# Kernel tuning notes

Hardware: AMD Instinct MI355X
Metric: run time of the kernel (lower is better)

The kernel has to match this reference:

```python
import jax, jax.numpy as jnp
import numpy as np

EPS = 1e-6
PC_MIN = jnp.array([-50.0, -50.0, -4.0], jnp.float32)
PC_MAX = jnp.array([50.0, 50.0, 4.0], jnp.float32)
IMG_H, IMG_W = 256, 704
G, P, L, D = 1, 8, 4, 128


def _conv3x3(x, w, b):
    y = jax.lax.conv_general_dilated(x, w, (1, 1), ((1, 1), (1, 1)),
                                     dimension_numbers=('NCHW', 'OIHW', 'NCHW'))
    return y + b[None, :, None, None]


def _inorm(x):
    # InstanceNorm2d(affine=False), eps=1e-5, per-sample per-channel over (H,W)
    m = jnp.mean(x, axis=(2, 3), keepdims=True)
    v = jnp.var(x, axis=(2, 3), keepdims=True)
    return (x - m) * jax.lax.rsqrt(v + 1e-5)


def _bilinear(img, xy):
    # img: [H, W, C]; xy: [M, 2] in [0,1] (align_corners=False, zero padding)
    H, W, _ = img.shape
    px = xy[:, 0] * W - 0.5
    py = xy[:, 1] * H - 0.5
    x0 = jnp.floor(px)
    y0 = jnp.floor(py)
    wx = px - x0
    wy = py - y0
    x0 = x0.astype(jnp.int32)
    y0 = y0.astype(jnp.int32)

    def tap(xi, yi, w):
        ok = (xi >= 0) & (xi < W) & (yi >= 0) & (yi < H)
        v = img[jnp.clip(yi, 0, H - 1), jnp.clip(xi, 0, W - 1)]
        return v * (w * ok)[:, None]

    return (tap(x0, y0, (1 - wx) * (1 - wy)) + tap(x0 + 1, y0, wx * (1 - wy)) +
            tap(x0, y0 + 1, (1 - wx) * wy) + tap(x0 + 1, y0 + 1, wx * wy))


def _sampling_4d(pts, feats, scale_w, l2i):
    # pts: [B,Q,G,P,3]; feats: list of [B*G,N,Hl,Wl,C]; scale_w: [B,Q,G,1,P,L]; l2i: [B,N,4,4]
    B, Q, g, p, _ = pts.shape
    N = l2i.shape[1]
    hom = jnp.concatenate([pts, jnp.ones(pts.shape[:-1] + (1,), pts.dtype)], -1)
    cam = jnp.einsum('bnij,bqgpj->bqngpi', l2i, hom)  # project to each camera
    z = cam[..., 2:3]
    xy = cam[..., :2] / jnp.maximum(z, 1e-5)
    xy = xy / jnp.array([IMG_W, IMG_H], xy.dtype)
    xy = jnp.where(z > 1e-5, xy, -1e4)  # behind camera -> samples zero
    xy = jnp.transpose(xy, (0, 3, 2, 1, 4, 5)).reshape(B * g * N, Q * p, 2)
    out = 0.0
    for l, f in enumerate(feats):
        C = f.shape[-1]
        fi = f.reshape(B * g * N, f.shape[2], f.shape[3], C)
        s = jax.vmap(_bilinear)(fi, xy).reshape(B, g, N, Q, p, C).sum(2)  # sum over cameras
        w = jnp.transpose(scale_w[:, :, :, 0, :, l], (0, 2, 1, 3))  # [B,G,Q,P]
        out = out + s * w[..., None]
    return jnp.transpose(out, (0, 2, 1, 3, 4))  # [B,Q,G,P,C]


def _forward(feat0, feat1, feat2, feat3, lidar2img, bev_query, bev_pos,
             in_w, in_b, off_w, off_b, sw_w, sw_b,
             pe_w1, pe_b1, pe_w2, pe_b2,
             mid_w1, mid_b1, mid_w2, mid_b2, mid_w3, mid_b3,
             out_w, out_b):
    B, _, h, w = bev_query.shape
    # decoder prologue: b n (g c) H W -> (b g) n H W c  (G=1)
    feats = [jnp.transpose(f, (0, 1, 3, 4, 2)) for f in (feat0, feat1, feat2, feat3)]
    q = _inorm(bev_query + _conv3x3(bev_query, in_w, in_b))
    qf = jnp.transpose(q, (0, 2, 3, 1)).reshape(B, h * w, D)
    # sampling offsets (1x1 conv as matmul), mode='grid', scale=1.0
    off = jax.nn.sigmoid(qf @ off_w.T + off_b).reshape(B, h * w, G, P, 3)
    lim_xy = 0.25 * 1.0 + EPS
    lim_z = 4.0 + EPS
    off = jnp.concatenate([off[..., :2] * 2 * lim_xy - lim_xy,
                           off[..., 2:3] * 2 * lim_z - lim_z], -1)
    ref = bev_pos.reshape(B, h * w, 1, 1, 3) * (PC_MAX - PC_MIN) + PC_MIN
    pts = ref + off  # [B,Q,G,P,3] in world coords
    sw = (qf @ sw_w.T + sw_b).reshape(B, h * w, G, P, L)[:, :, :, None]  # b q g 1 p l
    sw = jax.nn.softmax(sw, axis=-1)
    sampled = _sampling_4d(pts, feats, sw, lidar2img)  # [B,Q,G,P,128]
    ref_n = (pts - PC_MIN) / (PC_MAX - PC_MIN)
    pe = jax.nn.relu(ref_n @ pe_w1 + pe_b1) @ pe_w2 + pe_b2  # PositionalEncodingMap MLP
    sampled = sampled + pe
    # b (h w) g p c -> b (p g c) h w
    sf = jnp.transpose(sampled, (0, 3, 2, 4, 1)).reshape(B, P * G * 128, h, w)
    m = jax.nn.gelu(jnp.einsum('oi,bihw->bohw', mid_w1, sf) + mid_b1[None, :, None, None], approximate=False)
    m = jax.nn.gelu(jnp.einsum('oi,bihw->bohw', mid_w2, m) + mid_b2[None, :, None, None], approximate=False)
    m = jnp.einsum('oi,bihw->bohw', mid_w3, m) + mid_b3[None, :, None, None]
    q = _inorm(q + m)
    q = _inorm(q + _conv3x3(q, out_w, out_b))
    height = jnp.transpose(off[..., 2], (0, 2, 3, 1)).reshape(B, G, P, h, w)
    return q, height


def _lidar2img_np():
    mats = []
    K = np.array([[500., 0., IMG_W / 2, 0.],
                  [0., 500., IMG_H / 2, 0.],
                  [0., 0., 1., 0.],
                  [0., 0., 0., 1.]])
    for n in range(6):
        th = 2 * np.pi * n / 6
        fwd = np.array([np.cos(th), np.sin(th), 0.])
        right = np.array([-np.sin(th), np.cos(th), 0.])
        down = np.array([0., 0., -1.])
        R = np.stack([right, down, fwd])
        c = fwd * 0.5 + np.array([0., 0., 1.5])
        T = np.eye(4)
        T[:3, :3] = R
        T[:3, 3] = -R @ c
        mats.append(K @ T)
    return np.stack(mats)[None].astype(np.float32)


def setup_inputs():
    key = jax.random.key(0)
    ks = jax.random.split(key, 16)

    def rn(k, shape, s=0.02):
        return jax.random.normal(k, shape, jnp.float32) * s

    B, N, h, w = 1, 6, 128, 128
    return dict(
        feat0=jax.random.normal(ks[0], (B, N, 128, 32, 88), jnp.float32),
        feat1=jax.random.normal(ks[1], (B, N, 128, 16, 44), jnp.float32),
        feat2=jax.random.normal(ks[2], (B, N, 128, 8, 22), jnp.float32),
        feat3=jax.random.normal(ks[3], (B, N, 128, 4, 11), jnp.float32),
        lidar2img=jnp.asarray(_lidar2img_np()),
        bev_query=jax.random.normal(ks[4], (B, 128, h, w), jnp.float32),
        bev_pos=jax.random.uniform(ks[5], (B, h, w, 3), jnp.float32),
        in_w=rn(ks[6], (128, 128, 3, 3)), in_b=jnp.zeros(128, jnp.float32),
        off_w=rn(ks[7], (G * P * 3, 128)),
        off_b=jax.random.uniform(ks[8], (G * P * 3,), jnp.float32, -4.0, 4.0),
        sw_w=rn(ks[9], (G * P * L, 128)), sw_b=jnp.zeros(G * P * L, jnp.float32),
        pe_w1=rn(ks[10], (3, 256), 0.5), pe_b1=jnp.zeros(256, jnp.float32),
        pe_w2=rn(ks[11], (256, 128), 0.1), pe_b2=jnp.zeros(128, jnp.float32),
        mid_w1=rn(ks[12], (512, P * 128)), mid_b1=jnp.zeros(512, jnp.float32),
        mid_w2=rn(ks[13], (512, 512)), mid_b2=jnp.zeros(512, jnp.float32),
        mid_w3=rn(ks[14], (128, 512)), mid_b3=jnp.zeros(128, jnp.float32),
        out_w=rn(ks[15], (128, 128, 3, 3)), out_b=jnp.zeros(128, jnp.float32),
    )


def reference(feat0, feat1, feat2, feat3, lidar2img, bev_query, bev_pos,
              in_w, in_b, off_w, off_b, sw_w, sw_b,
              pe_w1, pe_b1, pe_w2, pe_b2,
              mid_w1, mid_b1, mid_w2, mid_b2, mid_w3, mid_b3,
              out_w, out_b):
    return _forward(feat0, feat1, feat2, feat3, lidar2img, bev_query, bev_pos,
                    in_w, in_b, off_w, off_b, sw_w, sw_b,
                    pe_w1, pe_b1, pe_w2, pe_b2,
                    mid_w1, mid_b1, mid_w2, mid_b2, mid_w3, mid_b3,
                    out_w, out_b)
```

## Files before the change

### kernel.cpp

```cpp
#include <hip/hip_runtime.h>
#include <hip/hip_bf16.h>
#include <math.h>

#define HW 16384

typedef __attribute__((ext_vector_type(8))) short short8;
typedef __attribute__((ext_vector_type(4))) float floatx4;
typedef __attribute__((ext_vector_type(2))) float floatx2;

__device__ __forceinline__ float gelu_exact(float x){
    return 0.5f * x * (1.0f + erff(x * 0.7071067811865475f));
}

__device__ __forceinline__ floatx2 bf2x(unsigned int u){
    floatx2 r;
    r.x = __uint_as_float(u << 16);
    r.y = __uint_as_float(u & 0xffff0000u);
    return r;
}

template<int CW, int HL, int WL>
__device__ __forceinline__ void ft_tile(
    float* tile, const float* __restrict__ in, __hip_bfloat16* __restrict__ out,
    int n, int y, int x0, int base, int t)
{
    const float* src = in + ((size_t)n * 128 * HL + y) * WL + x0;
    constexpr int NE = 128 * CW;
    for (int idx = t; idx < NE; idx += 256) {
        int c = idx / CW, x = idx - c * CW;
        tile[c * 45 + x] = src[(size_t)c * (HL * WL) + x];
    }
    __syncthreads();
    __hip_bfloat16* dst = out + base + ((size_t)(n * HL + y) * WL + x0) * 128;
    constexpr int NO = CW * 16;
    for (int idx = t; idx < NO; idx += 256) {
        int x = idx >> 4, g = idx & 15;
        union { __hip_bfloat16 h[8]; uint4 u; } pk;
        #pragma unroll
        for (int jj = 0; jj < 8; jj++)
            pk.h[jj] = __float2bfloat16(tile[(g * 8 + jj) * 45 + x]);
        *(uint4*)&dst[(size_t)x * 128 + g * 8] = pk.u;
    }
}

__global__ __launch_bounds__(256) void feat_transpose_all_k(
    const float* __restrict__ f0, const float* __restrict__ f1,
    const float* __restrict__ f2, const float* __restrict__ f3,
    __hip_bfloat16* __restrict__ out)
{
    __shared__ float tile[128 * 45];
    int b = blockIdx.x, t = threadIdx.x;
    if (b < 384) {
        int n = b >> 6, q = b & 63, y = q >> 1, x0 = (q & 1) * 44;
        ft_tile<44, 32, 88>(tile, f0, out, n, y, x0, 0, t);
    } else if (b < 480) {
        int r = b - 384, n = r >> 4, y = r & 15;
        ft_tile<44, 16, 44>(tile, f1, out, n, y, 0, 2162688, t);
    } else if (b < 528) {
        int r = b - 480, n = r >> 3, y = r & 7;
        ft_tile<22, 8, 22>(tile, f2, out, n, y, 0, 2703360, t);
    } else {
        int r = b - 528, n = r >> 2, y = r & 3;
        ft_tile<11, 4, 11>(tile, f3, out, n, y, 0, 2838528, t);
    }
}

__global__ __launch_bounds__(256) void prep_k(
    const float* __restrict__ mid_w1, const float* __restrict__ mid_w2,
    const float* __restrict__ mid_w3, const float* __restrict__ pe_w2,
    const float* __restrict__ off_w,  const float* __restrict__ off_b,
    const float* __restrict__ sw_w,   const float* __restrict__ sw_b,
    const float* __restrict__ in_w,   const float* __restrict__ out_w,
    __hip_bfloat16* __restrict__ Wb1, __hip_bfloat16* __restrict__ Wb2,
    __hip_bfloat16* __restrict__ Wb3, __hip_bfloat16* __restrict__ Wpe,
    __hip_bfloat16* __restrict__ Wof, float* __restrict__ Bof,
    __hip_bfloat16* __restrict__ Wcv1, __hip_bfloat16* __restrict__ Wcv2)
{
    int b = blockIdx.x, t = threadIdx.x;
    if (b < 2048) {
        int i = b * 256 + t; Wb1[i] = __float2bfloat16(mid_w1[i]);
    } else if (b < 3072) {
        int i = (b - 2048) * 256 + t; Wb2[i] = __float2bfloat16(mid_w2[i]);
    } else if (b < 3328) {
        int i = (b - 3072) * 256 + t; Wb3[i] = __float2bfloat16(mid_w3[i]);
    } else if (b < 3456) {
        int n = b - 3328; Wpe[n * 256 + t] = __float2bfloat16(pe_w2[t * 128 + n]);
    } else if (b < 3584) {
        int n = b - 3456;
        if (t < 128) {
            float w = 0.f;
            if (n < 24)      w = off_w[n * 128 + t];
            else if (n < 56) w = sw_w[(n - 24) * 128 + t];
            Wof[n * 128 + t] = __float2bfloat16(w);
            if (t == 0) Bof[n] = (n < 24) ? off_b[n] : ((n < 56) ? sw_b[n - 24] : 0.f);
        }
    } else if (b < 3712) {
        int o = b - 3584;
        for (int idx = t; idx < 1152; idx += 256) {
            int s = idx >> 7, i = idx & 127;
            Wcv1[o * 1152 + idx] = __float2bfloat16(in_w[(o * 128 + i) * 9 + s]);
        }
    } else {
        int o = b - 3712;
        for (int idx = t; idx < 1152; idx += 256) {
            int s = idx >> 7, i = idx & 127;
            Wcv2[o * 1152 + idx] = __float2bfloat16(out_w[(o * 128 + i) * 9 + s]);
        }
    }
}

__global__ __launch_bounds__(256) void chw2hwc_pad_k(
    const float* __restrict__ q, const float* __restrict__ stats,
    __hip_bfloat16* __restrict__ out)
{
    __shared__ float tile[128][65];
    __shared__ float sm[128], sr[128];
    int t = threadIdx.x;
    if (t < 128) {
        if (stats) {
            float s = stats[2 * t], s2 = stats[2 * t + 1];
            float mean = s * (1.0f / HW);
            sm[t] = mean;
            sr[t] = rsqrtf(s2 * (1.0f / HW) - mean * mean + 1e-5f);
        } else {
            sm[t] = 0.f; sr[t] = 1.f;
        }
    }
    int b = blockIdx.x;
    int y = b >> 1, x0 = (b & 1) * 64;
    int xi = t & 63, c0 = t >> 6;
    for (int c = c0; c < 128; c += 4)
        tile[c][xi] = q[c * HW + y * 128 + x0 + xi];
    __syncthreads();
    int xp = t >> 2, cg = (t & 3) * 32;
    __hip_bfloat16* dst = out + ((size_t)(y + 1) * 130 + (x0 + 1 + xp)) * 128;
    #pragma unroll
    for (int g = 0; g < 4; g++) {
        int c = cg + g * 8;
        union { __hip_bfloat16 h[8]; uint4 u; } pk;
        #pragma unroll
        for (int j = 0; j < 8; j++)
            pk.h[j] = __float2bfloat16((tile[c + j][xp] - sm[c + j]) * sr[c + j]);
        *(uint4*)&dst[c] = pk.u;
    }
}

template<int BM, int BN, int ACT, int OUTT, int CONV>
__global__ __launch_bounds__(256) void bgemm_k(
    const __hip_bfloat16* __restrict__ X, const __hip_bfloat16* __restrict__ W,
    const float* __restrict__ bias, void* __restrict__ outp,
    const float* __restrict__ res,
    const float* __restrict__ rstats, float* __restrict__ ostats,
    int M, int K, int N)
{
    constexpr int ROWS = BM + BN;
    constexpr int ITERS = (ROWS * 4) / 256;
    constexpr int BUFE  = ROWS * 32;
    constexpr int NBUF  = (ITERS == 2) ? 4 : 3;
    __shared__ __align__(16) __hip_bfloat16 SH[NBUF * BUFE];
    int t = threadIdx.x;
    int w = t >> 6, lane = t & 63;
    int mb = blockIdx.y * BM, nb = blockIdx.x * BN;
    int cy = mb >> 7, cx = mb & 127;
    constexpr int WM = BM / 2;
    constexpr int MI = WM / 16;
    constexpr int NJ = BN / 32;
    int wm = (w & 1) * WM, wn = (w >> 1) * (BN / 2);
    int lm = lane & 15, lq = lane >> 4;
    int sl = (lq ^ ((lm >> 1) & 3)) * 8;
    floatx4 zero = {0.f, 0.f, 0.f, 0.f};
    floatx4 acc[MI][NJ];
    #pragma unroll
    for (int i = 0; i < MI; i++)
        #pragma unroll
        for (int j = 0; j < NJ; j++) acc[i][j] = zero;

    const int nsteps = K >> 5;

    auto STAGE = [&](int bufi, int tk2) {
        int kb_ = tk2 * 32;
        int s_ = kb_ >> 7;
        int dyi_ = s_ / 3, dxi_ = s_ - dyi_ * 3;
        #pragma unroll
        for (int it = 0; it < ITERS; it++) {
            int chunk = it * 256 + t;
            int row = chunk >> 2;
            int ko = ((chunk & 3) ^ ((row >> 1) & 3)) * 8;
            const __hip_bfloat16* src;
            if (row < BM) {
                if (CONV)
                    src = X + (((size_t)(cy + dyi_) * 130) + (cx + dxi_ + row)) * 128 + (kb_ & 127) + ko;
                else
                    src = X + (size_t)(mb + row) * K + kb_ + ko;
            } else {
                src = W + (size_t)(nb + row - BM) * K + kb_ + ko;
            }
            __builtin_amdgcn_global_load_lds(
                (const __attribute__((address_space(1))) void*)src,
                (__attribute__((address_space(3))) void*)&SH[bufi * BUFE + (it * 256 + (t & ~63)) * 8],
                16, 0, 0);
        }
    };

    #pragma unroll
    for (int pi = 0; pi < NBUF - 1; pi++)
        if (pi < nsteps) STAGE(pi, pi);

    for (int tk = 0; tk < nsteps; ++tk) {
        int rem = nsteps - 1 - tk;
        if constexpr (ITERS == 2) {
            if (rem >= 2)      asm volatile("s_waitcnt vmcnt(4)" ::: "memory");
            else if (rem == 1) asm volatile("s_waitcnt vmcnt(2)" ::: "memory");
            else               asm volatile("s_waitcnt vmcnt(0)" ::: "memory");
        } else {
            if (rem >= 1)      asm volatile("s_waitcnt vmcnt(4)" ::: "memory");
            else               asm volatile("s_waitcnt vmcnt(0)" ::: "memory");
        }
        __builtin_amdgcn_s_barrier();
        int tkn = tk + NBUF - 1;
        if (tkn < nsteps) STAGE(tkn % NBUF, tkn);

        const __hip_bfloat16* As = SH + (tk % NBUF) * BUFE;
        const __hip_bfloat16* Bs = As + BM * 32;
        short8 af[MI], bf[NJ];
        #pragma unroll
        for (int i = 0; i < MI; i++)
            af[i] = *(const short8*)&As[(wm + i * 16 + lm) * 32 + sl];
        #pragma unroll
        for (int j = 0; j < NJ; j++)
            bf[j] = *(const short8*)&Bs[(wn + j * 16 + lm) * 32 + sl];
        #pragma unroll
        for (int i = 0; i < MI; i++)
            #pragma unroll
            for (int j = 0; j < NJ; j++)
                acc[i][j] = __builtin_amdgcn_mfma_f32_16x16x32_bf16(af[i], bf[j], acc[i][j], 0, 0, 0);
    }

    float invM = 1.0f / (float)M;
    #pragma unroll
    for (int j = 0; j < NJ; j++) {
        int n = nb + wn + j * 16 + lm;
        float bv = bias[n];
        float rmean = 0.f, rrstd = 0.f;
        if (OUTT == 1 && res && rstats) {
            float s = rstats[2 * n], s2 = rstats[2 * n + 1];
            rmean = s * invM;
            rrstd = rsqrtf(s2 * invM - rmean * rmean + 1e-5f);
        }
        float ss = 0.f, ss2 = 0.f;
        #pragma unroll
        for (int i = 0; i < MI; i++) {
            #pragma unroll
            for (int r = 0; r < 4; r++) {
                int m = mb + wm + i * 16 + lq * 4 + r;
                float v = acc[i][j][r] + bv;
                if (ACT) v = gelu_exact(v);
                if (OUTT == 0) {
                    ((__hip_bfloat16*)outp)[(size_t)m * N + n] = __float2bfloat16(v);
                } else {
                    if (res) {
                        float rv = res[(size_t)n * M + m];
                        v += rstats ? (rv - rmean) * rrstd : rv;
                    }
                    ((float*)outp)[(size_t)n * M + m] = v;
                    ss += v; ss2 += v * v;
                }
            }
        }
        if (OUTT == 1 && ostats) {
            ss  += __shfl_xor(ss, 16);  ss  += __shfl_xor(ss, 32);
            ss2 += __shfl_xor(ss2, 16); ss2 += __shfl_xor(ss2, 32);
            if (lq == 0) {
                atomicAdd(&ostats[2 * n], ss);
                atomicAdd(&ostats[2 * n + 1], ss2);
            }
        }
    }
}

__global__ __launch_bounds__(256) void pe_bgemm_k(
    const float* __restrict__ pts, const float* __restrict__ pe_w1,
    const float* __restrict__ pe_b1, const __hip_bfloat16* __restrict__ W,
    const float* __restrict__ bias, __hip_bfloat16* __restrict__ out)
{
    __shared__ __align__(16) __hip_bfloat16 As[128 * 32];
    __shared__ __align__(16) __hip_bfloat16 Bs[128 * 32];
    __shared__ __align__(16) float wps[4][256];
    int t = threadIdx.x;
    int w = t >> 6, lane = t & 63;
    int mb = blockIdx.x * 128;
    {
        int d = t >> 6, c = (t & 63) * 4;
        float4 v;
        if (d == 0) v = *(const float4*)&pe_b1[c];
        else        v = *(const float4*)&pe_w1[(d - 1) * 256 + c];
        *(float4*)&wps[d][c] = v;
    }
    int cg = t & 3;
    int r0 = t >> 2;
    float rn[2][3];
    #pragma unroll
    for (int h = 0; h < 2; h++) {
        int r = mb + r0 + h * 64;
        rn[h][0] = (pts[(size_t)r * 3 + 0] + 50.f) * 0.01f;
        rn[h][1] = (pts[(size_t)r * 3 + 1] + 50.f) * 0.01f;
        rn[h][2] = (pts[(size_t)r * 3 + 2] + 4.f) * 0.125f;
    }
    int wm = (w & 1) * 64, wn = (w >> 1) * 64;
    int lm = lane & 15, lq = lane >> 4;
    floatx4 zero = {0.f, 0.f, 0.f, 0.f};
    floatx4 acc[4][4];
    #pragma unroll
    for (int i = 0; i < 4; i++)
        #pragma unroll
        for (int j = 0; j < 4; j++) acc[i][j] = zero;
    for (int kb = 0; kb < 256; kb += 32) {
        __syncthreads();
        #pragma unroll
        for (int it = 0; it < 2; it++) {
            int chunk = it * 256 + t;
            int brow = chunk >> 2, ko = (chunk & 3) * 8;
            const __hip_bfloat16* src = W + (size_t)brow * 256 + kb + ko;
            __builtin_amdgcn_global_load_lds(
                (const __attribute__((address_space(1))) void*)src,
                (__attribute__((address_space(3))) void*)&Bs[(size_t)(it * 256 + (t & ~63)) * 8],
                16, 0, 0);
        }
        int c0 = kb + cg * 8;
        float4 bva = *(const float4*)&wps[0][c0], bvb = *(const float4*)&wps[0][c0 + 4];
        float4 wxa = *(const float4*)&wps[1][c0], wxb = *(const float4*)&wps[1][c0 + 4];
        float4 wya = *(const float4*)&wps[2][c0], wyb = *(const float4*)&wps[2][c0 + 4];
        float4 wza = *(const float4*)&wps[3][c0], wzb = *(const float4*)&wps[3][c0 + 4];
        #pragma unroll
        for (int h = 0; h < 2; h++) {
            const float* bv = (const float*)&bva;
            const float* wx = (const float*)&wxa;
            const float* wy = (const float*)&wya;
            const float* wz = (const float*)&wza;
            union { __hip_bfloat16 hh[8]; uint4 u; } pk;
            #pragma unroll
            for (int j = 0; j < 4; j++) {
                float v = bv[j] + rn[h][0] * wx[j] + rn[h][1] * wy[j] + rn[h][2] * wz[j];
                pk.hh[j] = __float2bfloat16(fmaxf(v, 0.f));
            }
            bv = (const float*)&bvb; wx = (const float*)&wxb;
            wy = (const float*)&wyb; wz = (const float*)&wzb;
            #pragma unroll
            for (int j = 0; j < 4; j++) {
                float v = bv[j] + rn[h][0] * wx[j] + rn[h][1] * wy[j] + rn[h][2] * wz[j];
                pk.hh[4 + j] = __float2bfloat16(fmaxf(v, 0.f));
            }
            *(uint4*)&As[(r0 + h * 64) * 32 + cg * 8] = pk.u;
        }
        __syncthreads();
        short8 af[4], bf[4];
        #pragma unroll
        for (int i = 0; i < 4; i++)
            af[i] = *(const short8*)&As[(wm + i * 16 + lm) * 32 + lq * 8];
        #pragma unroll
        for (int j = 0; j < 4; j++)
            bf[j] = *(const short8*)&Bs[(wn + j * 16 + lm) * 32 + lq * 8];
        #pragma unroll
        for (int i = 0; i < 4; i++)
            #pragma unroll
            for (int j = 0; j < 4; j++)
                acc[i][j] = __builtin_amdgcn_mfma_f32_16x16x32_bf16(af[i], bf[j], acc[i][j], 0, 0, 0);
    }
    #pragma unroll
    for (int i = 0; i < 4; i++) {
        #pragma unroll
        for (int j = 0; j < 4; j++) {
            int n = wn + j * 16 + lm;
            float bv = bias[n];
            #pragma unroll
            for (int r = 0; r < 4; r++) {
                int m = mb + wm + i * 16 + lq * 4 + r;
                out[(size_t)m * 128 + n] = __float2bfloat16(acc[i][j][r] + bv);
            }
        }
    }
}

__global__ __launch_bounds__(256) void inorm_apply_k(
    const float* __restrict__ in, const float* __restrict__ stats, float* __restrict__ out)
{
    int b = blockIdx.x;
    int c = b >> 3, seg = b & 7;
    float s = stats[2 * c], s2 = stats[2 * c + 1];
    float mean = s * (1.0f / HW);
    float rstd = rsqrtf(s2 * (1.0f / HW) - mean * mean + 1e-5f);
    const float4* pi = (const float4*)(in + (size_t)c * HW + seg * 2048);
    float4*       po = (float4*)(out + (size_t)c * HW + seg * 2048);
    int t = threadIdx.x;
    #pragma unroll
    for (int k = 0; k < 2; k++) {
        float4 v = pi[t + k * 256];
        v.x = (v.x - mean) * rstd; v.y = (v.y - mean) * rstd;
        v.z = (v.z - mean) * rstd; v.w = (v.w - mean) * rstd;
        po[t + k * 256] = v;
    }
}

__global__ __launch_bounds__(256) void offpost_k(
    const float* __restrict__ raw, const float* __restrict__ bev_pos,
    float* __restrict__ pts, float* __restrict__ swn, float* __restrict__ height_out)
{
    int pix = blockIdx.x * 256 + threadIdx.x;
    const float pcmin[3] = {-50.f, -50.f, -4.f};
    const float rng[3]   = {100.f, 100.f, 8.f};
    float bp[3];
    #pragma unroll
    for (int d = 0; d < 3; d++) bp[d] = bev_pos[pix * 3 + d];
    #pragma unroll
    for (int p = 0; p < 8; p++) {
        #pragma unroll
        for (int d = 0; d < 3; d++) {
            float acc = raw[(p * 3 + d) * HW + pix];
            float sv = 1.f / (1.f + expf(-acc));
            float lim = (d == 2) ? (4.0f + 1e-6f) : (0.25f + 1e-6f);
            float offv = sv * 2.f * lim - lim;
            float refv = bp[d] * rng[d] + pcmin[d];
            pts[pix * 24 + p * 3 + d] = refv + offv;
            if (d == 2) height_out[p * HW + pix] = offv;
        }
        float r[4], m = -1e30f;
        #pragma unroll
        for (int l = 0; l < 4; l++) {
            r[l] = raw[(24 + p * 4 + l) * HW + pix];
            m = fmaxf(m, r[l]);
        }
        float sum = 0.f;
        #pragma unroll
        for (int l = 0; l < 4; l++) { r[l] = expf(r[l] - m); sum += r[l]; }
        float inv = 1.f / sum;
        #pragma unroll
        for (int l = 0; l < 4; l++) swn[pix * 32 + p * 4 + l] = r[l] * inv;
    }
}

__global__ __launch_bounds__(512) void sample_k(
    const __hip_bfloat16* __restrict__ featT, const float* __restrict__ pts,
    const float* __restrict__ swn,   const float* __restrict__ l2i,
    __hip_bfloat16* __restrict__ sf)
{
    int bid = blockIdx.x;
    int pix = (bid & 7) * 2048 + (bid >> 3);
    int t = threadIdx.x;
    int lane = t & 63, wv = t >> 6;
    __shared__ float pts_s[24];
    __shared__ float swl_s[32];
    __shared__ float M[96];
    __shared__ __align__(16) int   offs[8][24][4];
    __shared__ __align__(16) float wts[8][24][4];
    __shared__ int cnt[8];
    if (t < 96) M[t] = l2i[t];
    if (t < 24) pts_s[t] = pts[pix * 24 + t];
    if (t < 32) swl_s[t] = swn[pix * 32 + t];
    if (t < 8)  cnt[t] = 0;
    __syncthreads();

    floatx2 acc;
    {
        unsigned int u = *(const unsigned int*)&sf[(size_t)pix * 1024 + wv * 128 + 2 * lane];
        acc = bf2x(u);
    }

    const int lHt[4] = {32, 16, 8, 4}, lWt[4] = {88, 44, 22, 11};
    const int loff[4] = {0, 2162688, 2703360, 2838528};
    if (t < 192) {
        int p = t / 24;
        int rr = t - p * 24;
        int n = rr >> 2, l = rr & 3;
        float X = pts_s[p * 3], Y = pts_s[p * 3 + 1], Z = pts_s[p * 3 + 2];
        const float* Mn = &M[n * 16];
        float zc = Mn[8] * X + Mn[9] * Y + Mn[10] * Z + Mn[11];
        if (zc > 1e-5f) {
            float inv = 1.f / zc;
            float xn = (Mn[0] * X + Mn[1] * Y + Mn[2] * Z + Mn[3]) * inv * (1.f / 704.f);
            float yn = (Mn[4] * X + Mn[5] * Y + Mn[6] * Z + Mn[7]) * inv * (1.f / 256.f);
            int Wl = lWt[l], Hl = lHt[l];
            float px = xn * Wl - 0.5f, py = yn * Hl - 0.5f;
            px = fminf(fmaxf(px, -2.f), (float)(Wl + 1));
            py = fminf(fmaxf(py, -2.f), (float)(Hl + 1));
            float x0f = floorf(px), y0f = floorf(py);
            float wx = px - x0f, wy = py - y0f;
            int x0 = (int)x0f, y0 = (int)y0f;
            bool xi0 = (unsigned)x0 < (unsigned)Wl, xi1 = (unsigned)(x0 + 1) < (unsigned)Wl;
            bool yi0 = (unsigned)y0 < (unsigned)Hl, yi1 = (unsigned)(y0 + 1) < (unsigned)Hl;
            if ((xi0 || xi1) && (yi0 || yi1)) {
                float wl = swl_s[p * 4 + l];
                float w00 = wl * (1.f - wx) * (1.f - wy) * (float)(xi0 && yi0);
                float w10 = wl * wx * (1.f - wy)         * (float)(xi1 && yi0);
                float w01 = wl * (1.f - wx) * wy         * (float)(xi0 && yi1);
                float w11 = wl * wx * wy                 * (float)(xi1 && yi1);
                int x0c = min(max(x0, 0), Wl - 1), x1c = min(max(x0 + 1, 0), Wl - 1);
                int y0c = min(max(y0, 0), Hl - 1), y1c = min(max(y0 + 1, 0), Hl - 1);
                int base = loff[l] + n * Hl * Wl * 128;
                int idx = atomicAdd(&cnt[p], 1);
                offs[p][idx][0] = (base + (y0c * Wl + x0c) * 128) * 2;
                offs[p][idx][1] = (base + (y0c * Wl + x1c) * 128) * 2;
                offs[p][idx][2] = (base + (y1c * Wl + x0c) * 128) * 2;
                offs[p][idx][3] = (base + (y1c * Wl + x1c) * 128) * 2;
                wts[p][idx][0] = w00; wts[p][idx][1] = w10;
                wts[p][idx][2] = w01; wts[p][idx][3] = w11;
            }
        }
    }
    __syncthreads();

    const char* fbase = (const char*)featT;
    int lane4 = lane * 4;
    {
        int p = wv;
        int np = cnt[p];
        floatx2 a0 = acc;
        floatx2 a1 = {0.f, 0.f};
        int j = 0;
        #pragma unroll 1
        for (; j + 2 <= np; j += 2) {
            int4   oA = *(const int4*)&offs[p][j][0];
            float4 wA = *(const float4*)&wts[p][j][0];
            int4   oB = *(const int4*)&offs[p][j + 1][0];
            float4 wB = *(const float4*)&wts[p][j + 1][0];
            unsigned int v0 = *(const unsigned int*)(fbase + (unsigned)(oA.x + lane4));
            unsigned int v1 = *(const unsigned int*)(fbase + (unsigned)(oA.y + lane4));
            unsigned int v2 = *(const unsigned int*)(fbase + (unsigned)(oA.z + lane4));
            unsigned int v3 = *(const unsigned int*)(fbase + (unsigned)(oA.w + lane4));
            unsigned int v4 = *(const unsigned int*)(fbase + (unsigned)(oB.x + lane4));
            unsigned int v5 = *(const unsigned int*)(fbase + (unsigned)(oB.y + lane4));
            unsigned int v6 = *(const unsigned int*)(fbase + (unsigned)(oB.z + lane4));
            unsigned int v7 = *(const unsigned int*)(fbase + (unsigned)(oB.w + lane4));
            a0 += bf2x(v0) * wA.x;
            a0 += bf2x(v1) * wA.y;
            a0 += bf2x(v2) * wA.z;
            a0 += bf2x(v3) * wA.w;
            a1 += bf2x(v4) * wB.x;
            a1 += bf2x(v5) * wB.y;
            a1 += bf2x(v6) * wB.z;
            a1 += bf2x(v7) * wB.w;
        }
        if (j < np) {
            int4   o = *(const int4*)&offs[p][j][0];
            float4 w = *(const float4*)&wts[p][j][0];
            unsigned int v0 = *(const unsigned int*)(fbase + (unsigned)(o.x + lane4));
            unsigned int v1 = *(const unsigned int*)(fbase + (unsigned)(o.y + lane4));
            unsigned int v2 = *(const unsigned int*)(fbase + (unsigned)(o.z + lane4));
            unsigned int v3 = *(const unsigned int*)(fbase + (unsigned)(o.w + lane4));
            a0 += bf2x(v0) * w.x;
            a0 += bf2x(v1) * w.y;
            a0 += bf2x(v2) * w.z;
            a0 += bf2x(v3) * w.w;
        }
        acc = a0 + a1;
    }
    {
        union { __hip_bfloat16 h[2]; unsigned int u; } pk;
        pk.h[0] = __float2bfloat16(acc.x);
        pk.h[1] = __float2bfloat16(acc.y);
        *(unsigned int*)&sf[(size_t)pix * 1024 + wv * 128 + 2 * lane] = pk.u;
    }
}

extern "C" void kernel_launch(void* const* d_in, const int* in_sizes, int n_in,
                              void* d_out, int out_size, void* d_ws, size_t ws_size,
                              hipStream_t stream)
{
    const float* feat[4] = {(const float*)d_in[0], (const float*)d_in[1],
                            (const float*)d_in[2], (const float*)d_in[3]};
    const float* l2i       = (const float*)d_in[4];
    const float* bev_query = (const float*)d_in[5];
    const float* bev_pos   = (const float*)d_in[6];
    const float* in_w  = (const float*)d_in[7];  const float* in_b  = (const float*)d_in[8];
    const float* off_w = (const float*)d_in[9];  const float* off_b = (const float*)d_in[10];
    const float* sw_w  = (const float*)d_in[11]; const float* sw_b  = (const float*)d_in[12];
    const float* pe_w1 = (const float*)d_in[13]; const float* pe_b1 = (const float*)d_in[14];
    const float* pe_w2 = (const float*)d_in[15]; const float* pe_b2 = (const float*)d_in[16];
    const float* mid_w1 = (const float*)d_in[17]; const float* mid_b1 = (const float*)d_in[18];
    const float* mid_w2 = (const float*)d_in[19]; const float* mid_b2 = (const float*)d_in[20];
    const float* mid_w3 = (const float*)d_in[21]; const float* mid_b3 = (const float*)d_in[22];
    const float* out_w  = (const float*)d_in[23]; const float* out_b  = (const float*)d_in[24];

    float* ws = (float*)d_ws;
    float* fTf = ws;
    __hip_bfloat16* fT = (__hip_bfloat16*)fTf;
    float* Bb  = fTf + 1436160;
    float* Cb  = Bb + 2097152;
    float* Gb  = Cb + 2097152;
    float* Dp  = Gb + 2097152;
    float* Eb  = Dp + 393216;
    float* QTf = Eb + 524288;
    __hip_bfloat16* qT = (__hip_bfloat16*)QTf;
    float* SFf = QTf + 1081600;
    __hip_bfloat16* sfb = (__hip_bfloat16*)SFf;
    float* M1f = SFf + 8388608;
    __hip_bfloat16* m1b = (__hip_bfloat16*)M1f;
    float* M2f = M1f + 4194304;
    __hip_bfloat16* m2b = (__hip_bfloat16*)M2f;
    float* WC1 = M2f + 4194304;
    __hip_bfloat16* Wcv1 = (__hip_bfloat16*)WC1;
    float* WC2 = WC1 + 73728;
    __hip_bfloat16* Wcv2 = (__hip_bfloat16*)WC2;
    float* W1f = WC2 + 73728;
    __hip_bfloat16* Wb1 = (__hip_bfloat16*)W1f;
    float* W2f = W1f + 262144;
    __hip_bfloat16* Wb2 = (__hip_bfloat16*)W2f;
    float* W3f = W2f + 131072;
    __hip_bfloat16* Wb3 = (__hip_bfloat16*)W3f;
    float* WPf = W3f + 32768;
    __hip_bfloat16* Wpe = (__hip_bfloat16*)WPf;
    float* WOf = WPf + 16384;
    __hip_bfloat16* Wof = (__hip_bfloat16*)WOf;
    float* Bof = WOf + 8192;
    float* Stats = Bof + 128;
    float* stats1 = Stats;
    float* stats2 = Stats + 256;
    float* stats3 = Stats + 512;

    float* q_out = (float*)d_out;
    float* h_out = q_out + 2097152;

    hipMemsetAsync(qT, 0, (size_t)130 * 130 * 128 * sizeof(__hip_bfloat16), stream);
    hipMemsetAsync(Stats, 0, 768 * sizeof(float), stream);

    feat_transpose_all_k<<<552, 256, 0, stream>>>(feat[0], feat[1], feat[2], feat[3], fT);
    prep_k<<<3840, 256, 0, stream>>>(mid_w1, mid_w2, mid_w3, pe_w2, off_w, off_b, sw_w, sw_b,
                                     in_w, out_w, Wb1, Wb2, Wb3, Wpe, Wof, Bof, Wcv1, Wcv2);

    chw2hwc_pad_k<<<256, 256, 0, stream>>>(bev_query, nullptr, qT);
    bgemm_k<64, 64, 0, 1, 1><<<dim3(2, 256), 256, 0, stream>>>(
        qT, Wcv1, in_b, Cb, bev_query, nullptr, stats1, HW, 1152, 128);

    chw2hwc_pad_k<<<256, 256, 0, stream>>>(Cb, stats1, qT);
    bgemm_k<64, 64, 0, 1, 1><<<dim3(2, 256), 256, 0, stream>>>(
        qT + 131 * 128, Wof, Bof, Bb, nullptr, nullptr, nullptr, HW, 128, 128);
    offpost_k<<<64, 256, 0, stream>>>(Bb, bev_pos, Dp, Eb, h_out);

    pe_bgemm_k<<<1024, 256, 0, stream>>>(Dp, pe_w1, pe_b1, Wpe, pe_b2, sfb);

    sample_k<<<HW, 512, 0, stream>>>(fT, Dp, Eb, l2i, sfb);

    bgemm_k<128, 128, 1, 0, 0><<<dim3(4, 128), 256, 0, stream>>>(
        sfb, Wb1, mid_b1, m1b, nullptr, nullptr, nullptr, HW, 1024, 512);
    bgemm_k<128, 128, 1, 0, 0><<<dim3(4, 128), 256, 0, stream>>>(
        m1b, Wb2, mid_b2, m2b, nullptr, nullptr, nullptr, HW, 512, 512);
    bgemm_k<64, 64, 0, 1, 0><<<dim3(2, 256), 256, 0, stream>>>(
        m2b, Wb3, mid_b3, Bb, Cb, stats1, stats2, HW, 512, 128);

    chw2hwc_pad_k<<<256, 256, 0, stream>>>(Bb, stats2, qT);
    bgemm_k<64, 64, 0, 1, 1><<<dim3(2, 256), 256, 0, stream>>>(
        qT, Wcv2, out_b, Gb, Bb, stats2, stats3, HW, 1152, 128);
    inorm_apply_k<<<1024, 256, 0, stream>>>(Gb, stats3, q_out);
}
```

Before: 404.0 us.

## Merge setup kernels and memsets, widen offpost grid, halve sample_k block size

Merges the feature transpose, weight preparation, border-only zeroing of the padded query buffer and stats clearing into one setup kernel, replacing two memsets and two launches. offpost_k now spreads the 8 sampling points across 4x more blocks to raise parallelism. sample_k drops to 256 threads, with each wave handling two points serially, and uses a linear pixel order in place of the interleaved one. Zeroing only the pad border depends on every later writer of qT covering the interior, and the smaller sample blocks change occupancy and latency hiding.

```diff
diff --git a/kernel.cpp b/kernel.cpp
--- a/kernel.cpp
+++ b/kernel.cpp
@@ -43,29 +43,10 @@
     }
 }
 
-__global__ __launch_bounds__(256) void feat_transpose_all_k(
+__global__ __launch_bounds__(256) void setup_k(
     const float* __restrict__ f0, const float* __restrict__ f1,
     const float* __restrict__ f2, const float* __restrict__ f3,
-    __hip_bfloat16* __restrict__ out)
-{
-    __shared__ float tile[128 * 45];
-    int b = blockIdx.x, t = threadIdx.x;
-    if (b < 384) {
-        int n = b >> 6, q = b & 63, y = q >> 1, x0 = (q & 1) * 44;
-        ft_tile<44, 32, 88>(tile, f0, out, n, y, x0, 0, t);
-    } else if (b < 480) {
-        int r = b - 384, n = r >> 4, y = r & 15;
-        ft_tile<44, 16, 44>(tile, f1, out, n, y, 0, 2162688, t);
-    } else if (b < 528) {
-        int r = b - 480, n = r >> 3, y = r & 7;
-        ft_tile<22, 8, 22>(tile, f2, out, n, y, 0, 2703360, t);
-    } else {
-        int r = b - 528, n = r >> 2, y = r & 3;
-        ft_tile<11, 4, 11>(tile, f3, out, n, y, 0, 2838528, t);
-    }
-}
-
-__global__ __launch_bounds__(256) void prep_k(
+    __hip_bfloat16* __restrict__ fT,
     const float* __restrict__ mid_w1, const float* __restrict__ mid_w2,
     const float* __restrict__ mid_w3, const float* __restrict__ pe_w2,
     const float* __restrict__ off_w,  const float* __restrict__ off_b,
@@ -74,19 +55,33 @@
     __hip_bfloat16* __restrict__ Wb1, __hip_bfloat16* __restrict__ Wb2,
     __hip_bfloat16* __restrict__ Wb3, __hip_bfloat16* __restrict__ Wpe,
     __hip_bfloat16* __restrict__ Wof, float* __restrict__ Bof,
-    __hip_bfloat16* __restrict__ Wcv1, __hip_bfloat16* __restrict__ Wcv2)
-{
+    __hip_bfloat16* __restrict__ Wcv1, __hip_bfloat16* __restrict__ Wcv2,
+    __hip_bfloat16* __restrict__ qTo, float* __restrict__ Stats)
+{
+    __shared__ float tile[128 * 45];
     int b = blockIdx.x, t = threadIdx.x;
-    if (b < 2048) {
-        int i = b * 256 + t; Wb1[i] = __float2bfloat16(mid_w1[i]);
-    } else if (b < 3072) {
-        int i = (b - 2048) * 256 + t; Wb2[i] = __float2bfloat16(mid_w2[i]);
-    } else if (b < 3328) {
-        int i = (b - 3072) * 256 + t; Wb3[i] = __float2bfloat16(mid_w3[i]);
-    } else if (b < 3456) {
-        int n = b - 3328; Wpe[n * 256 + t] = __float2bfloat16(pe_w2[t * 128 + n]);
-    } else if (b < 3584) {
-        int n = b - 3456;
+    if (b < 384) {
+        int n = b >> 6, q = b & 63, y = q >> 1, x0 = (q & 1) * 44;
+        ft_tile<44, 32, 88>(tile, f0, fT, n, y, x0, 0, t);
+    } else if (b < 480) {
+        int r = b - 384, n = r >> 4, y = r & 15;
+        ft_tile<44, 16, 44>(tile, f1, fT, n, y, 0, 2162688, t);
+    } else if (b < 528) {
+        int r = b - 480, n = r >> 3, y = r & 7;
+        ft_tile<22, 8, 22>(tile, f2, fT, n, y, 0, 2703360, t);
+    } else if (b < 552) {
+        int r = b - 528, n = r >> 2, y = r & 3;
+        ft_tile<11, 4, 11>(tile, f3, fT, n, y, 0, 2838528, t);
+    } else if (b < 2600) {
+        int i = (b - 552) * 256 + t; Wb1[i] = __float2bfloat16(mid_w1[i]);
+    } else if (b < 3624) {
+        int i = (b - 2600) * 256 + t; Wb2[i] = __float2bfloat16(mid_w2[i]);
+    } else if (b < 3880) {
+        int i = (b - 3624) * 256 + t; Wb3[i] = __float2bfloat16(mid_w3[i]);
+    } else if (b < 4008) {
+        int n = b - 3880; Wpe[n * 256 + t] = __float2bfloat16(pe_w2[t * 128 + n]);
+    } else if (b < 4136) {
+        int n = b - 4008;
         if (t < 128) {
             float w = 0.f;
             if (n < 24)      w = off_w[n * 128 + t];
@@ -94,18 +89,35 @@
             Wof[n * 128 + t] = __float2bfloat16(w);
             if (t == 0) Bof[n] = (n < 24) ? off_b[n] : ((n < 56) ? sw_b[n - 24] : 0.f);
         }
-    } else if (b < 3712) {
-        int o = b - 3584;
+    } else if (b < 4264) {
+        int o = b - 4136;
         for (int idx = t; idx < 1152; idx += 256) {
             int s = idx >> 7, i = idx & 127;
             Wcv1[o * 1152 + idx] = __float2bfloat16(in_w[(o * 128 + i) * 9 + s]);
         }
-    } else {
-        int o = b - 3712;
+    } else if (b < 4392) {
+        int o = b - 4264;
         for (int idx = t; idx < 1152; idx += 256) {
             int s = idx >> 7, i = idx & 127;
             Wcv2[o * 1152 + idx] = __float2bfloat16(out_w[(o * 128 + i) * 9 + s]);
         }
+    } else if (b < 4425) {
+        int g = (b - 4392) * 256 + t;
+        if (g < 8256) {
+            int pixi = g >> 4, part = g & 15;
+            int row, col;
+            if (pixi < 130)      { row = 0;   col = pixi; }
+            else if (pixi < 260) { row = 129; col = pixi - 130; }
+            else {
+                int r = pixi - 260;
+                row = 1 + (r & 127);
+                col = (r < 128) ? 0 : 129;
+            }
+            uint4 z = {0u, 0u, 0u, 0u};
+            *(uint4*)&qTo[((size_t)row * 130 + col) * 128 + part * 8] = z;
+        }
+    } else {
+        Stats[t] = 0.f; Stats[256 + t] = 0.f; Stats[512 + t] = 0.f;
     }
 }
 
@@ -405,14 +417,17 @@
     const float* __restrict__ raw, const float* __restrict__ bev_pos,
     float* __restrict__ pts, float* __restrict__ swn, float* __restrict__ height_out)
 {
-    int pix = blockIdx.x * 256 + threadIdx.x;
+    int b = blockIdx.x;
+    int pix = (b & 63) * 256 + threadIdx.x;
+    int p0 = (b >> 6) * 2;
     const float pcmin[3] = {-50.f, -50.f, -4.f};
     const float rng[3]   = {100.f, 100.f, 8.f};
     float bp[3];
     #pragma unroll
     for (int d = 0; d < 3; d++) bp[d] = bev_pos[pix * 3 + d];
     #pragma unroll
-    for (int p = 0; p < 8; p++) {
+    for (int pi = 0; pi < 2; pi++) {
+        int p = p0 + pi;
         #pragma unroll
         for (int d = 0; d < 3; d++) {
             float acc = raw[(p * 3 + d) * HW + pix];
@@ -438,13 +453,12 @@
     }
 }
 
-__global__ __launch_bounds__(512) void sample_k(
+__global__ __launch_bounds__(256) void sample_k(
     const __hip_bfloat16* __restrict__ featT, const float* __restrict__ pts,
     const float* __restrict__ swn,   const float* __restrict__ l2i,
     __hip_bfloat16* __restrict__ sf)
 {
-    int bid = blockIdx.x;
-    int pix = (bid & 7) * 2048 + (bid >> 3);
+    int pix = blockIdx.x;
     int t = threadIdx.x;
     int lane = t & 63, wv = t >> 6;
     __shared__ float pts_s[24];
@@ -459,10 +473,11 @@
     if (t < 8)  cnt[t] = 0;
     __syncthreads();
 
-    floatx2 acc;
-    {
-        unsigned int u = *(const unsigned int*)&sf[(size_t)pix * 1024 + wv * 128 + 2 * lane];
-        acc = bf2x(u);
+    floatx2 acc[2];
+    #pragma unroll
+    for (int i = 0; i < 2; i++) {
+        unsigned int u = *(const unsigned int*)&sf[(size_t)pix * 1024 + (wv * 2 + i) * 128 + 2 * lane];
+        acc[i] = bf2x(u);
     }
 
     const int lHt[4] = {32, 16, 8, 4}, lWt[4] = {88, 44, 22, 11};
@@ -510,10 +525,11 @@
 
     const char* fbase = (const char*)featT;
     int lane4 = lane * 4;
-    {
-        int p = wv;
+    #pragma unroll
+    for (int i = 0; i < 2; i++) {
+        int p = wv * 2 + i;
         int np = cnt[p];
-        floatx2 a0 = acc;
+        floatx2 a0 = acc[i];
         floatx2 a1 = {0.f, 0.f};
         int j = 0;
         #pragma unroll 1
@@ -551,13 +567,14 @@
             a0 += bf2x(v2) * w.z;
             a0 += bf2x(v3) * w.w;
         }
-        acc = a0 + a1;
-    }
-    {
+        acc[i] = a0 + a1;
+    }
+    #pragma unroll
+    for (int i = 0; i < 2; i++) {
         union { __hip_bfloat16 h[2]; unsigned int u; } pk;
-        pk.h[0] = __float2bfloat16(acc.x);
-        pk.h[1] = __float2bfloat16(acc.y);
-        *(unsigned int*)&sf[(size_t)pix * 1024 + wv * 128 + 2 * lane] = pk.u;
+        pk.h[0] = __float2bfloat16(acc[i].x);
+        pk.h[1] = __float2bfloat16(acc[i].y);
+        *(unsigned int*)&sf[(size_t)pix * 1024 + (wv * 2 + i) * 128 + 2 * lane] = pk.u;
     }
 }
 
@@ -619,12 +636,10 @@
     float* q_out = (float*)d_out;
     float* h_out = q_out + 2097152;
 
-    hipMemsetAsync(qT, 0, (size_t)130 * 130 * 128 * sizeof(__hip_bfloat16), stream);
-    hipMemsetAsync(Stats, 0, 768 * sizeof(float), stream);
-
-    feat_transpose_all_k<<<552, 256, 0, stream>>>(feat[0], feat[1], feat[2], feat[3], fT);
-    prep_k<<<3840, 256, 0, stream>>>(mid_w1, mid_w2, mid_w3, pe_w2, off_w, off_b, sw_w, sw_b,
-                                     in_w, out_w, Wb1, Wb2, Wb3, Wpe, Wof, Bof, Wcv1, Wcv2);
+    setup_k<<<4426, 256, 0, stream>>>(feat[0], feat[1], feat[2], feat[3], fT,
+                                      mid_w1, mid_w2, mid_w3, pe_w2, off_w, off_b, sw_w, sw_b,
+                                      in_w, out_w, Wb1, Wb2, Wb3, Wpe, Wof, Bof, Wcv1, Wcv2,
+                                      qT, Stats);
 
     chw2hwc_pad_k<<<256, 256, 0, stream>>>(bev_query, nullptr, qT);
     bgemm_k<64, 64, 0, 1, 1><<<dim3(2, 256), 256, 0, stream>>>(
@@ -633,11 +648,11 @@
     chw2hwc_pad_k<<<256, 256, 0, stream>>>(Cb, stats1, qT);
     bgemm_k<64, 64, 0, 1, 1><<<dim3(2, 256), 256, 0, stream>>>(
         qT + 131 * 128, Wof, Bof, Bb, nullptr, nullptr, nullptr, HW, 128, 128);
-    offpost_k<<<64, 256, 0, stream>>>(Bb, bev_pos, Dp, Eb, h_out);
+    offpost_k<<<256, 256, 0, stream>>>(Bb, bev_pos, Dp, Eb, h_out);
 
     pe_bgemm_k<<<1024, 256, 0, stream>>>(Dp, pe_w1, pe_b1, Wpe, pe_b2, sfb);
 
-    sample_k<<<HW, 512, 0, stream>>>(fT, Dp, Eb, l2i, sfb);
+    sample_k<<<HW, 256, 0, stream>>>(fT, Dp, Eb, l2i, sfb);
 
     bgemm_k<128, 128, 1, 0, 0><<<dim3(4, 128), 256, 0, stream>>>(
         sfb, Wb1, mid_b1, m1b, nullptr, nullptr, nullptr, HW, 1024, 512);
```

New measurement: 378.4 us. 6.3% less time.
